# Optimization experiments

Measured on AMD Instinct MI355X. Metric: run time of the kernel, lower is better.

## Reference

```python
import jax, jax.numpy as jnp
import numpy as np

EPS = 1e-6
BN_EPS = 1e-5


def thomas(a, b, c, d):
    # a,b,c,d: (R, N) batched tridiagonal systems, solved along axis 1.
    aT, bT, cT, dT = a.T, b.T, c.T, d.T  # (N, R)
    z = jnp.zeros((a.shape[0],), a.dtype)

    def fwd_step(carry, row):
        cp, dp = carry
        ai, bi, ci, di = row
        denom = bi - ai * cp + EPS
        cs = ci / denom
        ds = (di - ai * dp) / denom
        return (cs, ds), (cs, ds)

    _, (c_star, d_star) = jax.lax.scan(fwd_step, (z, z), (aT, bT, cT, dT))

    def bwd_step(x_next, row):
        cs, ds = row
        x = ds - cs * x_next
        return x, x

    x_last = d_star[-1]
    _, xs = jax.lax.scan(bwd_step, x_last, (c_star[:-1], d_star[:-1]), reverse=True)
    return jnp.concatenate([xs, x_last[None]], axis=0).T  # (R, N)


def thomas_diffuse(d, coeff):
    a = -coeff
    c = -coeff
    b = 1.0 + 2.0 * coeff
    b = b.at[:, 0].set(1.0 + coeff[:, 0])
    b = b.at[:, -1].set(1.0 + coeff[:, -1])
    return thomas(a, b, c, d)


def diffusion_layer(u, alpha_base, beta_base, alpha_tc, beta_tc, mix, dt, num_steps, dx=1.0, dy=1.0):
    B, C, H, W = u.shape
    t = 0.0
    for _ in range(num_steps):
        alpha = jnp.clip(alpha_base + alpha_tc * t, EPS, 10.0)
        u = jnp.einsum('cd,bdhw->bchw', mix, u)
        coeff_x = jnp.broadcast_to(alpha, (B, C, H, W)).reshape(B * C * H, W) * (dt / 2) / dx ** 2
        u = thomas_diffuse(u.reshape(B * C * H, W), coeff_x).reshape(B, C, H, W)
        t += dt / 2
        beta = jnp.clip(beta_base + beta_tc * t, EPS, 10.0)
        coeff_y = jnp.broadcast_to(beta, (B, C, H, W)).transpose(0, 1, 3, 2).reshape(B * C * W, H) * (dt / 2) / dy ** 2
        u_t = u.transpose(0, 1, 3, 2).reshape(B * C * W, H)
        u = thomas_diffuse(u_t, coeff_y).reshape(B, C, W, H).transpose(0, 1, 3, 2)
        t += dt / 2
    return u


def symmetric(Y, K, gamma, beta):
    # F_sym(Y) = -K^T relu(BN(K Y)); nn.Linear computes Y @ K.T
    B = Y.shape[0]
    Yf = Y.reshape(B, -1)
    KY = Yf @ K.T
    mean = jnp.mean(KY, axis=0)
    var = jnp.var(KY, axis=0)  # biased, like torch BN
    KYn = (KY - mean) / jnp.sqrt(var + BN_EPS) * gamma + beta
    s = jax.nn.relu(KYn)
    return (-(s @ K)).reshape(Y.shape)


def setup_inputs() -> dict:
    B, C, S = 64, 3, 48
    F = C * S * S
    key = jax.random.key(0)
    ks = jax.random.split(key, 8)
    x = jax.random.normal(ks[0], (B, C, S, S), dtype=jnp.float32)
    eyeC = jnp.eye(C, dtype=jnp.float32)
    eyeF = jnp.eye(F, dtype=jnp.float32)
    inp = {
        'x': x,
        'ab1': jnp.ones((C, S, S), jnp.float32),
        'bb1': jnp.ones((C, S, S), jnp.float32),
        'atc1': jnp.zeros((C, S, S), jnp.float32),
        'btc1': jnp.zeros((C, S, S), jnp.float32),
        'mix1': eyeC + 0.01 * jax.random.normal(ks[1], (C, C), jnp.float32),
        'ab2': jnp.ones((C, S, S), jnp.float32),
        'bb2': jnp.ones((C, S, S), jnp.float32),
        'atc2': jnp.zeros((C, S, S), jnp.float32),
        'btc2': jnp.zeros((C, S, S), jnp.float32),
        'mix2': eyeC + 0.01 * jax.random.normal(ks[2], (C, C), jnp.float32),
        'Kp': eyeF + 0.01 * jax.random.normal(ks[3], (F, F), jnp.float32),
        'gp': jnp.ones((F,), jnp.float32),
        'bp': jnp.zeros((F,), jnp.float32),
        'Ky': eyeF + 0.01 * jax.random.normal(ks[4], (F, F), jnp.float32),
        'gy': jnp.ones((F,), jnp.float32),
        'by_': jnp.zeros((F,), jnp.float32),
        'Kz': eyeF + 0.01 * jax.random.normal(ks[5], (F, F), jnp.float32),
        'gz': jnp.ones((F,), jnp.float32),
        'bz': jnp.zeros((F,), jnp.float32),
        'cw': jnp.ones((4,), jnp.float32) / 4.0,
        'fng': jnp.ones((3,), jnp.float32),
        'fnb': jnp.zeros((3,), jnp.float32),
    }
    return inp


def reference(x, ab1, bb1, atc1, btc1, mix1, ab2, bb2, atc2, btc2, mix2,
              Kp, gp, bp, Ky, gy, by_, Kz, gz, bz, cw, fng, fnb):
    d1 = diffusion_layer(x, ab1, bb1, atc1, btc1, mix1, 0.001, 8)
    d2 = diffusion_layer(x, ab2, bb2, atc2, btc2, mix2, 0.002, 5)
    # Parabolic block: Y <- Y + dt * F_sym(Y), dt=0.5, 4 steps
    Yp = x
    for _ in range(4):
        Yp = Yp + 0.5 * symmetric(Yp, Kp, gp, bp)
    # Hamiltonian block: dt=0.8, 3 steps
    Yh = x
    Zh = jnp.zeros_like(x)
    for _ in range(3):
        Yh = Yh + 0.8 * (-symmetric(Zh, Ky, gy, by_))
        Zh = Zh - 0.8 * symmetric(Yh, Kz, gz, bz)
    w = jax.nn.softmax(cw)
    combined = w[0] * d1 + w[1] * d2 + w[2] * Yp + w[3] * Yh
    mean = jnp.mean(combined, axis=(0, 2, 3), keepdims=True)
    var = jnp.var(combined, axis=(0, 2, 3), keepdims=True)
    combined = (combined - mean) / jnp.sqrt(var + BN_EPS) * fng[None, :, None, None] + fnb[None, :, None, None]
    return (combined, d1, d2, Yp, Yh)
```

## Files before the change

kernel.cpp:

```cpp
#include <hip/hip_runtime.h>
#include <cstdint>
#include <cstddef>

static constexpr int F      = 6912;
static constexpr int BATCH  = 64;
static constexpr size_t NF  = (size_t)BATCH * F;
static constexpr int BKT    = 64;
static constexpr int NT     = F / BKT;
static constexpr int NTH    = NT / 2;
static constexpr int NT2    = F / 32;
static constexpr int DEPTH  = 6;
static constexpr int PREF   = 4;
static constexpr int STAGE_B = 12288;
static constexpr int STAGE_U = STAGE_B / 2;
static constexpr size_t GEMM_LDS = 2 * (size_t)DEPTH * STAGE_B + 1024;

typedef short bf16x8 __attribute__((ext_vector_type(8)));
typedef float f32x4  __attribute__((ext_vector_type(4)));
typedef unsigned short ushort_t;

__device__ __forceinline__ unsigned short f2bf(float f) {
    union { float f; uint32_t u; } x; x.f = f;
    uint32_t r = x.u + 0x7fffu + ((x.u >> 16) & 1u);
    return (unsigned short)(r >> 16);
}

#define GLOAD_LDS16(gp, lp) \
    __builtin_amdgcn_global_load_lds((const __attribute__((address_space(1))) void*)(gp), \
                                     (__attribute__((address_space(3))) void*)(lp), 16, 0, 0)


__global__ __launch_bounds__(256) void build_ep3(
    const float* __restrict__ K0, const float* __restrict__ K1, const float* __restrict__ K2,
    ushort_t* __restrict__ P10, ushort_t* __restrict__ P20,
    ushort_t* __restrict__ P11, ushort_t* __restrict__ P21,
    ushort_t* __restrict__ P12, ushort_t* __restrict__ P22) {
    __shared__ float tile[64][65];
    int z = blockIdx.z;
    const float* K = (z == 0) ? K0 : (z == 1) ? K1 : K2;
    ushort_t* P1 = (z == 0) ? P10 : (z == 1) ? P11 : P12;
    ushort_t* P2 = (z == 0) ? P20 : (z == 1) ? P21 : P22;
    int bj = blockIdx.x * 64;
    int bi = blockIdx.y * 64;
    int t = threadIdx.x;
    int r = t >> 2, c0 = (t & 3) * 16;
    const float4* src = reinterpret_cast<const float4*>(K + (size_t)(bi + r) * F + bj + c0);
    float4 v0 = src[0], v1 = src[1], v2 = src[2], v3 = src[3];
    float vv[16] = {v0.x,v0.y,v0.z,v0.w, v1.x,v1.y,v1.z,v1.w,
                    v2.x,v2.y,v2.z,v2.w, v3.x,v3.y,v3.z,v3.w};
#pragma unroll
    for (int e = 0; e < 16; ++e) {
        float f = vv[e];
        if (bi + r == bj + c0 + e) f -= 1.0f;
        tile[r][c0 + e] = f;
    }
    __syncthreads();
#pragma unroll
    for (int i = 0; i < 2; ++i) {
        int g = t + i * 256;
        int rq = g >> 3, c8 = g & 7;
        ushort_t pk[8];
#pragma unroll
        for (int e = 0; e < 8; ++e) pk[e] = f2bf(tile[rq][c8 * 8 + e]);
        size_t nt = (size_t)((bi + rq) >> 5);
        size_t dst = ((nt * 108 + (bj >> 6)) * 32 + (rq & 31)) * 64 + c8 * 8;
        *reinterpret_cast<uint4*>(P1 + dst) = *reinterpret_cast<uint4*>(pk);
    }
#pragma unroll
    for (int i = 0; i < 2; ++i) {
        int g = t + i * 256;
        int rq = g >> 3, c8 = g & 7;
        ushort_t pk[8];
#pragma unroll
        for (int e = 0; e < 8; ++e) pk[e] = f2bf(tile[c8 * 8 + e][rq]);
        size_t nt = (size_t)((bj + rq) >> 5);
        size_t dst = ((nt * 108 + (bi >> 6)) * 32 + (rq & 31)) * 64 + c8 * 8;
        *reinterpret_cast<uint4*>(P2 + dst) = *reinterpret_cast<uint4*>(pk);
    }
}

__device__ __forceinline__ void issue_stage(const ushort_t* __restrict__ Abf,
                                            const ushort_t* __restrict__ EP,
                                            ushort_t* ring, int sidx,
                                            int nt_blk, int kt, int wl, int l) {
    int k0 = kt * BKT;
    ushort_t* bufA = ring + sidx * STAGE_U;
    ushort_t* bufB = bufA + 4096;
#pragma unroll
    for (int i = 0; i < 2; ++i) {
        int slot = wl * 128 + i * 64 + l;
        int row = slot >> 3;
        int cs16 = (slot & 7) ^ (row & 7);
        GLOAD_LDS16(Abf + (size_t)row * F + k0 + cs16 * 8, bufA + (wl * 128 + i * 64) * 8);
    }
    {
        const ushort_t* bbase = EP + ((size_t)nt_blk * 108 + kt) * 2048;
        int slot = wl * 64 + l;
        int row = slot >> 3;
        int cs16 = (slot & 7) ^ (row & 7);
        GLOAD_LDS16(bbase + row * 64 + cs16 * 8, bufB + (wl * 64) * 8);
    }
}

__device__ __forceinline__ void compute_stage(const ushort_t* ring, int sidx,
                                              f32x4 acc[2], int wl, int l) {
    const char* base = (const char*)(ring + sidx * STAGE_U);
    int lrow = l & 15, lq = l >> 4;
    int arow = wl * 16 + lrow;
#pragma unroll
    for (int ks = 0; ks < 2; ++ks) {
        int acol = ((ks * 4 + lq) ^ (arow & 7)) * 16;
        bf16x8 af = *(const bf16x8*)(base + arow * 128 + acol);
#pragma unroll
        for (int j = 0; j < 2; ++j) {
            int brow = j * 16 + lrow;
            int bcol = ((ks * 4 + lq) ^ (brow & 7)) * 16;
            bf16x8 bf = *(const bf16x8*)(base + 8192 + brow * 128 + bcol);
            acc[j] = __builtin_amdgcn_mfma_f32_16x16x32_bf16(af, bf, acc[j], 0, 0, 0);
        }
    }
}

template<int MODE>
__global__ __launch_bounds__(512) void gemm_fused(
    const ushort_t* __restrict__ Abf, const ushort_t* __restrict__ EP,
    const float* __restrict__ base_f32,
    const float* __restrict__ s_in,
    const float* __restrict__ gamma, const float* __restrict__ beta,
    float scale,
    float* __restrict__ out_f32, ushort_t* __restrict__ out_bf)
{
    extern __shared__ __align__(16) char smem[];
    ushort_t* stage = (ushort_t*)smem;
    float* redS = (float*)(smem + 2 * DEPTH * STAGE_B);
    float* redQ = redS + 128;

    int nt_blk = blockIdx.x;
    int n0 = nt_blk * 32;
    int tid = threadIdx.x;
    int w = tid >> 6, l = tid & 63;
    int wl = w & 3;
    int g  = w >> 2;
    ushort_t* ring = stage + g * (DEPTH * STAGE_U);
    int kbase = g * NTH;

    f32x4 acc[2];
    acc[0] = (f32x4)0.0f; acc[1] = (f32x4)0.0f;

#pragma unroll
    for (int t = 0; t < PREF; ++t) issue_stage(Abf, EP, ring, t, nt_blk, kbase + t, wl, l);

    for (int t = 0; t < NTH; ++t) {
        if (t + PREF < NTH) issue_stage(Abf, EP, ring, (t + PREF) % DEPTH, nt_blk, kbase + t + PREF, wl, l);
        int ahead = NTH - 1 - t; if (ahead > PREF) ahead = PREF;
        if (ahead >= 4)      asm volatile("s_waitcnt vmcnt(12)" ::: "memory");
        else if (ahead == 3) asm volatile("s_waitcnt vmcnt(9)"  ::: "memory");
        else if (ahead == 2) asm volatile("s_waitcnt vmcnt(6)"  ::: "memory");
        else if (ahead == 1) asm volatile("s_waitcnt vmcnt(3)"  ::: "memory");
        else                 asm volatile("s_waitcnt vmcnt(0)"  ::: "memory");
        __builtin_amdgcn_s_barrier();
        asm volatile("" ::: "memory");
        compute_stage(ring, t % DEPTH, acc, wl, l);
    }

    __syncthreads();
    float* accx = (float*)smem;
    if (w >= 4) {
        int base = ((w - 4) * 64 + l) * 8;
#pragma unroll
        for (int r = 0; r < 4; ++r) { accx[base + r] = acc[0][r]; accx[base + 4 + r] = acc[1][r]; }
    }
    __syncthreads();
    if (w < 4) {
        int base = (w * 64 + l) * 8;
#pragma unroll
        for (int r = 0; r < 4; ++r) { acc[0][r] += accx[base + r]; acc[1][r] += accx[base + 4 + r]; }
    }

    int lrow = l & 15, lq = l >> 4;
    if (MODE == 0) {
        float v[2][4];
        if (w < 4) {
#pragma unroll
            for (int j = 0; j < 2; ++j)
#pragma unroll
                for (int r = 0; r < 4; ++r) {
                    int m = w * 16 + lq * 4 + r;
                    int n = n0 + j * 16 + lrow;
                    v[j][r] = acc[j][r] + base_f32[(size_t)m * F + n];
                }
#pragma unroll
            for (int j = 0; j < 2; ++j) {
                float ps = v[j][0] + v[j][1] + v[j][2] + v[j][3];
                float pq = v[j][0]*v[j][0] + v[j][1]*v[j][1] + v[j][2]*v[j][2] + v[j][3]*v[j][3];
                ps += __shfl_xor(ps, 16); pq += __shfl_xor(pq, 16);
                ps += __shfl_xor(ps, 32); pq += __shfl_xor(pq, 32);
                if (lq == 0) { redS[(w * 2 + j) * 16 + lrow] = ps; redQ[(w * 2 + j) * 16 + lrow] = pq; }
            }
        }
        __syncthreads();
        if (w < 4) {
#pragma unroll
            for (int j = 0; j < 2; ++j) {
                float ts = redS[(0*2+j)*16+lrow] + redS[(1*2+j)*16+lrow] + redS[(2*2+j)*16+lrow] + redS[(3*2+j)*16+lrow];
                float tq = redQ[(0*2+j)*16+lrow] + redQ[(1*2+j)*16+lrow] + redQ[(2*2+j)*16+lrow] + redQ[(3*2+j)*16+lrow];
                float mn = ts * (1.f / 64.f);
                float vr = tq * (1.f / 64.f) - mn * mn;
                int n = n0 + j * 16 + lrow;
                float inv = rsqrtf(vr + 1e-5f) * gamma[n];
                float bet = beta[n];
#pragma unroll
                for (int r = 0; r < 4; ++r) {
                    int m = w * 16 + lq * 4 + r;
                    float sv = fmaxf((v[j][r] - mn) * inv + bet, 0.f);
                    out_f32[(size_t)m * F + n] = sv;
                    out_bf[(size_t)m * F + n] = f2bf(sv);
                }
            }
        }
    } else {
        if (w < 4) {
#pragma unroll
            for (int j = 0; j < 2; ++j)
#pragma unroll
                for (int r = 0; r < 4; ++r) {
                    int m = w * 16 + lq * 4 + r;
                    int n = n0 + j * 16 + lrow;
                    size_t o = (size_t)m * F + n;
                    float ov = base_f32[o] + scale * (s_in[o] + acc[j][r]);
                    out_f32[o] = ov;
                    out_bf[o] = f2bf(ov);
                }
        }
    }
}

__global__ __launch_bounds__(256) void cvt_bf(const float* __restrict__ in, ushort_t* __restrict__ out) {
    size_t i = ((size_t)blockIdx.x * 256 + threadIdx.x) * 4;
    float4 v = *reinterpret_cast<const float4*>(in + i);
    ushort_t p[4] = { f2bf(v.x), f2bf(v.y), f2bf(v.z), f2bf(v.w) };
    *reinterpret_cast<uint2*>(out + i) = *reinterpret_cast<uint2*>(p);
}

__global__ __launch_bounds__(256) void transpose_coeff(
    const float* __restrict__ b1, const float* __restrict__ t1,
    const float* __restrict__ b2, const float* __restrict__ t2,
    float* __restrict__ o) {
    int idx = blockIdx.x * 256 + threadIdx.x;
    if (idx >= 4 * 6912) return;
    int a = idx / 6912, rem = idx % 6912;
    int c = rem / 2304, r2 = rem % 2304, wq = r2 / 48, k = r2 % 48;
    const float* src = (a == 0) ? b1 : (a == 1) ? t1 : (a == 2) ? b2 : t2;
    o[idx] = src[c * 2304 + k * 48 + wq];
}

__device__ __forceinline__ void thomas_row(float* up, int stride,
                                           const float* __restrict__ cb,
                                           const float* __restrict__ ct,
                                           float tcur, float dt2) {
    float cov[48], ur[48];
#pragma unroll
    for (int k = 0; k < 48; ++k)
        cov[k] = fminf(fmaxf(cb[k] + ct[k] * tcur, 1e-6f), 10.f) * dt2;
#pragma unroll
    for (int k = 0; k < 48; ++k) ur[k] = up[k * stride];
    float cp = 0.f, dp = 0.f;
#pragma unroll
    for (int k = 0; k < 48; ++k) {
        float co = cov[k];
        float bd = (k == 0 || k == 47) ? (1.f + co) : (1.f + 2.f * co);
        float den = bd + co * cp + 1e-6f;
        float rin = __builtin_amdgcn_rcpf(den);
        float cs = -co * rin;
        float ds = (ur[k] + co * dp) * rin;
        cov[k] = cs; ur[k] = ds; cp = cs; dp = ds;
    }
    float xv = ur[47];
#pragma unroll
    for (int k = 46; k >= 0; --k) { xv = ur[k] - cov[k] * xv; ur[k] = xv; }
#pragma unroll
    for (int k = 0; k < 48; ++k) up[k * stride] = ur[k];
}

__global__ __launch_bounds__(192) void diffusion_kern(
    const float* __restrict__ x,
    const float* __restrict__ ab1, const float* __restrict__ atc1,
    const float* __restrict__ ab2, const float* __restrict__ atc2,
    const float* __restrict__ btr,
    const float* __restrict__ mix1, const float* __restrict__ mix2,
    float* __restrict__ out1, float* __restrict__ out2)
{
    int blk = blockIdx.x;
    bool second = blk >= 64;
    int b = blk & 63;
    const float* ab  = second ? ab2  : ab1;
    const float* atc = second ? atc2 : atc1;
    const float* bbT = btr + (second ? 13824 : 0);
    const float* btT = btr + (second ? 20736 : 6912);
    const float* mx  = second ? mix2 : mix1;
    float dt = second ? 0.002f : 0.001f;
    int nsteps = second ? 5 : 8;
    float* out = second ? out2 : out1;

    __shared__ float u[3][48][49];
    int t = threadIdx.x;
    for (int idx = t; idx < 6912; idx += 192) {
        int c = idx / 2304, rem = idx % 2304;
        u[c][rem / 48][rem % 48] = x[(size_t)b * 6912 + idx];
    }
    float m00 = mx[0], m01 = mx[1], m02 = mx[2];
    float m10 = mx[3], m11 = mx[4], m12 = mx[5];
    float m20 = mx[6], m21 = mx[7], m22 = mx[8];
    __syncthreads();
    float tcur = 0.f, dt2 = dt * 0.5f;
    int cc = t / 48, rc = t % 48;
    for (int step = 0; step < nsteps; ++step) {
        float v0[12], v1[12], v2[12];
#pragma unroll
        for (int j = 0; j < 12; ++j) {
            int p = t + j * 192;
            int h = p / 48, wq = p % 48;
            v0[j] = u[0][h][wq]; v1[j] = u[1][h][wq]; v2[j] = u[2][h][wq];
        }
        __syncthreads();
#pragma unroll
        for (int j = 0; j < 12; ++j) {
            int p = t + j * 192;
            int h = p / 48, wq = p % 48;
            u[0][h][wq] = m00 * v0[j] + m01 * v1[j] + m02 * v2[j];
            u[1][h][wq] = m10 * v0[j] + m11 * v1[j] + m12 * v2[j];
            u[2][h][wq] = m20 * v0[j] + m21 * v1[j] + m22 * v2[j];
        }
        __syncthreads();
        if (t < 144)
            thomas_row(&u[cc][rc][0], 1, ab + (cc * 48 + rc) * 48, atc + (cc * 48 + rc) * 48, tcur, dt2);
        __syncthreads();
        tcur += dt2;
        if (t < 144)
            thomas_row(&u[cc][0][rc], 49, bbT + (cc * 48 + rc) * 48, btT + (cc * 48 + rc) * 48, tcur, dt2);
        __syncthreads();
        tcur += dt2;
    }
    for (int idx = t; idx < 6912; idx += 192) {
        int c = idx / 2304, rem = idx % 2304;
        out[(size_t)b * 6912 + idx] = u[c][rem / 48][rem % 48];
    }
}

__global__ __launch_bounds__(256) void combine_pass1(
    const float* __restrict__ cw,
    const float* __restrict__ d1, const float* __restrict__ d2,
    const float* __restrict__ yp, const float* __restrict__ yh,
    float* __restrict__ comb, float* __restrict__ stats)
{
    float c0 = cw[0], c1 = cw[1], c2 = cw[2], c3 = cw[3];
    float mxv = fmaxf(fmaxf(c0, c1), fmaxf(c2, c3));
    float e0 = expf(c0 - mxv), e1 = expf(c1 - mxv), e2 = expf(c2 - mxv), e3 = expf(c3 - mxv);
    float es = e0 + e1 + e2 + e3;
    float w0 = e0 / es, w1 = e1 / es, w2 = e2 / es, w3 = e3 / es;
    size_t base = (size_t)blockIdx.x * 1024;
    float ls[3] = {0.f, 0.f, 0.f}, lq[3] = {0.f, 0.f, 0.f};
#pragma unroll
    for (int j = 0; j < 4; ++j) {
        size_t idx = base + threadIdx.x + j * 256;
        float v = w0 * d1[idx] + w1 * d2[idx] + w2 * yp[idx] + w3 * yh[idx];
        comb[idx] = v;
        int c = (int)((idx / 2304) % 3);
        if (c == 0)      { ls[0] += v; lq[0] += v * v; }
        else if (c == 1) { ls[1] += v; lq[1] += v * v; }
        else             { ls[2] += v; lq[2] += v * v; }
    }
    __shared__ float bsum[6];
    if (threadIdx.x < 6) bsum[threadIdx.x] = 0.f;
    __syncthreads();
#pragma unroll
    for (int c = 0; c < 3; ++c) {
        atomicAdd(&bsum[c], ls[c]);
        atomicAdd(&bsum[3 + c], lq[c]);
    }
    __syncthreads();
    if (threadIdx.x < 6) atomicAdd(&stats[threadIdx.x], bsum[threadIdx.x]);
}

__global__ __launch_bounds__(256) void combine_pass2(
    const float* __restrict__ comb, const float* __restrict__ stats,
    const float* __restrict__ fng, const float* __restrict__ fnb,
    float* __restrict__ out0)
{
    const float inv_n = 1.f / 147456.f;
    size_t base = (size_t)blockIdx.x * 1024;
#pragma unroll
    for (int j = 0; j < 4; ++j) {
        size_t idx = base + threadIdx.x + j * 256;
        int c = (int)((idx / 2304) % 3);
        float mean = stats[c] * inv_n;
        float var = stats[3 + c] * inv_n - mean * mean;
        out0[idx] = (comb[idx] - mean) * rsqrtf(var + 1e-5f) * fng[c] + fnb[c];
    }
}

static constexpr size_t EB  = (size_t)F * F * 2;
static constexpr size_t NF4 = NF * 4;
static constexpr size_t WS_NEED = 6 * EB + 12 * NF4 + 2 * (NF * 2) + (1 << 20);

static void* g_ws = nullptr;
namespace {
struct WsInit {
    WsInit() { if (hipMalloc(&g_ws, WS_NEED) != hipSuccess) g_ws = nullptr; }
};
WsInit g_wsinit;
}

extern "C" void kernel_launch(void* const* d_in, const int* in_sizes, int n_in,
                              void* d_out, int out_size, void* d_ws, size_t ws_size,
                              hipStream_t stream)
{
    const float* x    = (const float*)d_in[0];
    const float* ab1  = (const float*)d_in[1];
    const float* bb1  = (const float*)d_in[2];
    const float* atc1 = (const float*)d_in[3];
    const float* btc1 = (const float*)d_in[4];
    const float* mix1 = (const float*)d_in[5];
    const float* ab2  = (const float*)d_in[6];
    const float* bb2  = (const float*)d_in[7];
    const float* atc2 = (const float*)d_in[8];
    const float* btc2 = (const float*)d_in[9];
    const float* mix2 = (const float*)d_in[10];
    const float* Kp   = (const float*)d_in[11];
    const float* gp   = (const float*)d_in[12];
    const float* bp   = (const float*)d_in[13];
    const float* Ky   = (const float*)d_in[14];
    const float* gy   = (const float*)d_in[15];
    const float* by_  = (const float*)d_in[16];
    const float* Kz   = (const float*)d_in[17];
    const float* gz   = (const float*)d_in[18];
    const float* bz   = (const float*)d_in[19];
    const float* cw   = (const float*)d_in[20];
    const float* fng  = (const float*)d_in[21];
    const float* fnb  = (const float*)d_in[22];

    float* out   = (float*)d_out;
    float* o_cmb = out;
    float* o_d1  = out + NF;
    float* o_d2  = out + 2 * NF;
    float* o_yp  = out + 3 * NF;
    float* o_yh  = out + 4 * NF;

    char* wsb = (ws_size >= WS_NEED) ? (char*)d_ws : (char*)g_ws;
    if (!wsb) wsb = (char*)d_ws;

    char* p = wsb;
    auto bump = [&](size_t bytes) { char* r = p; p += (bytes + 255) & ~(size_t)255; return r; };
    ushort_t* P1p = (ushort_t*)bump(EB);
    ushort_t* P2p = (ushort_t*)bump(EB);
    ushort_t* P1y = (ushort_t*)bump(EB);
    ushort_t* P2y = (ushort_t*)bump(EB);
    ushort_t* P1z = (ushort_t*)bump(EB);
    ushort_t* P2z = (ushort_t*)bump(EB);
    float* sbuf  = (float*)bump(NF4);
    ushort_t* s_bf = (ushort_t*)bump(NF * 2);
    ushort_t* Abf  = (ushort_t*)bump(NF * 2);
    float* Z0f  = (float*)bump(NF4);
    float* Y1   = (float*)bump(NF4);
    float* Y2   = (float*)bump(NF4);
    float* Y3   = (float*)bump(NF4);
    float* Yh1  = (float*)bump(NF4);
    float* Z1   = (float*)bump(NF4);
    float* Yh2  = (float*)bump(NF4);
    float* Z2   = (float*)bump(NF4);
    float* comb = (float*)bump(NF4);
    float* stats = (float*)bump(256);
    float* btr   = (float*)bump(4 * 6912 * 4);

    hipMemsetAsync(stats, 0, 32, stream);
    hipMemsetAsync(Z0f, 0, NF4, stream);

    transpose_coeff<<<108, 256, 0, stream>>>(bb1, btc1, bb2, btc2, btr);
    diffusion_kern<<<128, 192, 0, stream>>>(x, ab1, atc1, ab2, atc2, btr, mix1, mix2, o_d1, o_d2);

    build_ep3<<<dim3(108, 108, 3), 256, 0, stream>>>(Kp, Ky, Kz, P1p, P2p, P1y, P2y, P1z, P2z);

    cvt_bf<<<432, 256, 0, stream>>>(x, Abf);

    auto sym = [&](const float* A1, const ushort_t* P1, const ushort_t* P2,
                   const float* g, const float* bt, const float* Obase,
                   float sc, float* Onew) {
        gemm_fused<0><<<NT2, 512, GEMM_LDS, stream>>>(Abf, P1, A1, nullptr, g, bt, 0.f, sbuf, s_bf);
        gemm_fused<1><<<NT2, 512, GEMM_LDS, stream>>>(s_bf, P2, Obase, sbuf, nullptr, nullptr, sc, Onew, Abf);
    };

    sym(x,  P1p, P2p, gp, bp, x,  -0.5f, Y1);
    sym(Y1, P1p, P2p, gp, bp, Y1, -0.5f, Y2);
    sym(Y2, P1p, P2p, gp, bp, Y2, -0.5f, Y3);
    sym(Y3, P1p, P2p, gp, bp, Y3, -0.5f, o_yp);

    hipMemsetAsync(Abf, 0, NF * 2, stream);
    sym(Z0f, P1y, P2y, gy, by_, x,   0.8f, Yh1);
    sym(Yh1, P1z, P2z, gz, bz,  Z0f, 0.8f, Z1);
    sym(Z1,  P1y, P2y, gy, by_, Yh1, 0.8f, Yh2);
    sym(Yh2, P1z, P2z, gz, bz,  Z1,  0.8f, Z2);
    sym(Z2,  P1y, P2y, gy, by_, Yh2, 0.8f, o_yh);

    combine_pass1<<<432, 256, 0, stream>>>(cw, o_d1, o_d2, o_yp, o_yh, comb, stats);
    combine_pass2<<<432, 256, 0, stream>>>(comb, stats, fng, fnb, o_cmb);
}
```

Measured before the change: 775.5 us.

## Batch parabolic and Hamiltonian GEMM chains into shared two-chain launches

```diff
diff --git a/kernel.cpp b/kernel.cpp
--- a/kernel.cpp
+++ b/kernel.cpp
@@ -123,17 +123,30 @@
 
 template<int MODE>
 __global__ __launch_bounds__(512) void gemm_fused(
-    const ushort_t* __restrict__ Abf, const ushort_t* __restrict__ EP,
-    const float* __restrict__ base_f32,
-    const float* __restrict__ s_in,
-    const float* __restrict__ gamma, const float* __restrict__ beta,
-    float scale,
-    float* __restrict__ out_f32, ushort_t* __restrict__ out_bf)
+    const ushort_t* __restrict__ Abf0, const ushort_t* __restrict__ EP0,
+    const float* __restrict__ base0, const float* __restrict__ sin0,
+    const float* __restrict__ g0, const float* __restrict__ bt0, float sc0,
+    float* __restrict__ of0, ushort_t* __restrict__ ob0,
+    const ushort_t* __restrict__ Abf1, const ushort_t* __restrict__ EP1c,
+    const float* __restrict__ base1, const float* __restrict__ sin1,
+    const float* __restrict__ g1, const float* __restrict__ bt1, float sc1,
+    float* __restrict__ of1, ushort_t* __restrict__ ob1)
 {
     extern __shared__ __align__(16) char smem[];
     ushort_t* stage = (ushort_t*)smem;
     float* redS = (float*)(smem + 2 * DEPTH * STAGE_B);
     float* redQ = redS + 128;
+
+    int chain = blockIdx.y;
+    const ushort_t* Abf    = chain ? Abf1 : Abf0;
+    const ushort_t* EP     = chain ? EP1c : EP0;
+    const float* base_f32  = chain ? base1 : base0;
+    const float* s_in      = chain ? sin1 : sin0;
+    const float* gamma     = chain ? g1 : g0;
+    const float* beta      = chain ? bt1 : bt0;
+    float scale            = chain ? sc1 : sc0;
+    float* out_f32         = chain ? of1 : of0;
+    ushort_t* out_bf       = chain ? ob1 : ob0;
 
     int nt_blk = blockIdx.x;
     int n0 = nt_blk * 32;
@@ -401,7 +414,7 @@
 
 static constexpr size_t EB  = (size_t)F * F * 2;
 static constexpr size_t NF4 = NF * 4;
-static constexpr size_t WS_NEED = 6 * EB + 12 * NF4 + 2 * (NF * 2) + (1 << 20);
+static constexpr size_t WS_NEED = 6 * EB + 14 * NF4 + 4 * (NF * 2) + (1 << 20);
 
 static void* g_ws = nullptr;
 namespace {
@@ -457,9 +470,12 @@
     ushort_t* P2y = (ushort_t*)bump(EB);
     ushort_t* P1z = (ushort_t*)bump(EB);
     ushort_t* P2z = (ushort_t*)bump(EB);
-    float* sbuf  = (float*)bump(NF4);
-    ushort_t* s_bf = (ushort_t*)bump(NF * 2);
-    ushort_t* Abf  = (ushort_t*)bump(NF * 2);
+    float* sbuf_p = (float*)bump(NF4);
+    float* sbuf_h = (float*)bump(NF4);
+    ushort_t* sbf_p = (ushort_t*)bump(NF * 2);
+    ushort_t* sbf_h = (ushort_t*)bump(NF * 2);
+    ushort_t* Abf_p = (ushort_t*)bump(NF * 2);
+    ushort_t* Abf_h = (ushort_t*)bump(NF * 2);
     float* Z0f  = (float*)bump(NF4);
     float* Y1   = (float*)bump(NF4);
     float* Y2   = (float*)bump(NF4);
@@ -474,32 +490,38 @@
 
     hipMemsetAsync(stats, 0, 32, stream);
     hipMemsetAsync(Z0f, 0, NF4, stream);
+    hipMemsetAsync(Abf_h, 0, NF * 2, stream);
 
     transpose_coeff<<<108, 256, 0, stream>>>(bb1, btc1, bb2, btc2, btr);
     diffusion_kern<<<128, 192, 0, stream>>>(x, ab1, atc1, ab2, atc2, btr, mix1, mix2, o_d1, o_d2);
 
     build_ep3<<<dim3(108, 108, 3), 256, 0, stream>>>(Kp, Ky, Kz, P1p, P2p, P1y, P2y, P1z, P2z);
 
-    cvt_bf<<<432, 256, 0, stream>>>(x, Abf);
-
-    auto sym = [&](const float* A1, const ushort_t* P1, const ushort_t* P2,
-                   const float* g, const float* bt, const float* Obase,
-                   float sc, float* Onew) {
-        gemm_fused<0><<<NT2, 512, GEMM_LDS, stream>>>(Abf, P1, A1, nullptr, g, bt, 0.f, sbuf, s_bf);
-        gemm_fused<1><<<NT2, 512, GEMM_LDS, stream>>>(s_bf, P2, Obase, sbuf, nullptr, nullptr, sc, Onew, Abf);
+    cvt_bf<<<432, 256, 0, stream>>>(x, Abf_p);
+
+    auto step2 = [&](const float* A1p, const float* Obp, float* Onp,
+                     const ushort_t* P1h, const ushort_t* P2h,
+                     const float* gh, const float* bth,
+                     const float* A1h, const float* Obh, float* Onh) {
+        gemm_fused<0><<<dim3(NT2, 2), 512, GEMM_LDS, stream>>>(
+            Abf_p, P1p, A1p, nullptr, gp, bp, 0.f, sbuf_p, sbf_p,
+            Abf_h, P1h, A1h, nullptr, gh, bth, 0.f, sbuf_h, sbf_h);
+        gemm_fused<1><<<dim3(NT2, 2), 512, GEMM_LDS, stream>>>(
+            sbf_p, P2p, Obp, sbuf_p, nullptr, nullptr, -0.5f, Onp, Abf_p,
+            sbf_h, P2h, Obh, sbuf_h, nullptr, nullptr, 0.8f, Onh, Abf_h);
     };
 
-    sym(x,  P1p, P2p, gp, bp, x,  -0.5f, Y1);
-    sym(Y1, P1p, P2p, gp, bp, Y1, -0.5f, Y2);
-    sym(Y2, P1p, P2p, gp, bp, Y2, -0.5f, Y3);
-    sym(Y3, P1p, P2p, gp, bp, Y3, -0.5f, o_yp);
-
-    hipMemsetAsync(Abf, 0, NF * 2, stream);
-    sym(Z0f, P1y, P2y, gy, by_, x,   0.8f, Yh1);
-    sym(Yh1, P1z, P2z, gz, bz,  Z0f, 0.8f, Z1);
-    sym(Z1,  P1y, P2y, gy, by_, Yh1, 0.8f, Yh2);
-    sym(Yh2, P1z, P2z, gz, bz,  Z1,  0.8f, Z2);
-    sym(Z2,  P1y, P2y, gy, by_, Yh2, 0.8f, o_yh);
+    step2(x,  x,  Y1,   P1y, P2y, gy, by_, Z0f, x,   Yh1);
+    step2(Y1, Y1, Y2,   P1z, P2z, gz, bz,  Yh1, Z0f, Z1);
+    step2(Y2, Y2, Y3,   P1y, P2y, gy, by_, Z1,  Yh1, Yh2);
+    step2(Y3, Y3, o_yp, P1z, P2z, gz, bz,  Yh2, Z1,  Z2);
+
+    gemm_fused<0><<<dim3(NT2, 1), 512, GEMM_LDS, stream>>>(
+        Abf_h, P1y, Z2, nullptr, gy, by_, 0.f, sbuf_h, sbf_h,
+        nullptr, nullptr, nullptr, nullptr, nullptr, nullptr, 0.f, nullptr, nullptr);
+    gemm_fused<1><<<dim3(NT2, 1), 512, GEMM_LDS, stream>>>(
+        sbf_h, P2y, Yh2, sbuf_h, nullptr, nullptr, 0.8f, o_yh, Abf_h,
+        nullptr, nullptr, nullptr, nullptr, nullptr, nullptr, 0.f, nullptr, nullptr);
 
     combine_pass1<<<432, 256, 0, stream>>>(cw, o_d1, o_d2, o_yp, o_yh, comb, stats);
     combine_pass2<<<432, 256, 0, stream>>>(comb, stats, fng, fnb, o_cmb);
```

New measurement: 808.2 us. 1.04x slower.
